# Kernel optimization log

Hardware: AMD Instinct MI355X
Metric: run time of the kernel (lower is better)

Reference implementation:

```python
import jax, jax.numpy as jnp
import numpy as np

B, T, E, H = 64, 256, 300, 512        # batch, longest_sequence, embed dim, hidden
V, NTAGS, NCLS, DFF = 50000, 17, 18, 256  # vocab, universal POS tags, output classes, dense hidden


def setup_inputs() -> dict:
    key = jax.random.key(0)
    ks = jax.random.split(key, 11)
    su = 1.0 / np.sqrt(H)  # PyTorch LSTMCell/Linear uniform init scale
    return {
        "tokens": jax.random.randint(ks[0], (B, T), 0, V),
        "tags": jax.random.randint(ks[1], (T,), 0, NTAGS),
        "emb": jax.random.normal(ks[2], (V, E), jnp.float32),
        "W_ih": jax.random.uniform(ks[3], (NTAGS, 4 * H, E), jnp.float32, -su, su),
        "W_hh": jax.random.uniform(ks[4], (NTAGS, 4 * H, H), jnp.float32, -su, su),
        "b_ih": jax.random.uniform(ks[5], (NTAGS, 4 * H), jnp.float32, -su, su),
        "b_hh": jax.random.uniform(ks[6], (NTAGS, 4 * H), jnp.float32, -su, su),
        "W1": jax.random.uniform(ks[7], (DFF, H), jnp.float32, -su, su),
        "b1": jax.random.uniform(ks[8], (DFF,), jnp.float32, -su, su),
        "W2": jax.random.uniform(ks[9], (NCLS, DFF), jnp.float32, -1.0 / np.sqrt(DFF), 1.0 / np.sqrt(DFF)),
        "b2": jax.random.uniform(ks[10], (NCLS,), jnp.float32, -1.0 / np.sqrt(DFF), 1.0 / np.sqrt(DFF)),
    }


def reference(tokens, tags, emb, W_ih, W_hh, b_ih, b_hh, W1, b1, W2, b2):
    x = emb[tokens]                     # [B, T, E] embedding lookup
    xs = jnp.swapaxes(x, 0, 1)          # [T, B, E] time-major for scan

    def step(carry, inp):
        h, c = carry
        xt, tag = inp                   # xt: [B, E], tag: scalar int routing the cell
        gates = (xt @ W_ih[tag].T + h @ W_hh[tag].T
                 + b_ih[tag] + b_hh[tag])            # [B, 4H]
        i, f, g, o = jnp.split(gates, 4, axis=-1)    # PyTorch LSTMCell gate order
        i = jax.nn.sigmoid(i)
        f = jax.nn.sigmoid(f)
        g = jnp.tanh(g)
        o = jax.nn.sigmoid(o)
        c = f * c + i * g
        h = o * jnp.tanh(c)
        return (h, c), None

    h0 = jnp.zeros((x.shape[0], H), x.dtype)
    (h, _), _ = jax.lax.scan(step, (h0, h0), (xs, tags))
    # dense head: Linear -> ReLU -> (Dropout inactive at eval) -> Linear
    hid = jax.nn.relu(h @ W1.T + b1)
    return hid @ W2.T + b2              # [B, NCLS] multiclass logits
```

## Files before the change

kernel.cpp:

```cpp
#include <hip/hip_runtime.h>
#include <cstdint>
#include <cstddef>

#define BB   64
#define TT   256
#define EE   300
#define HH   512
#define G4H  2048
#define NCLS 18
#define DFF  256
#define NBLK 256

__device__ __forceinline__ float fast_exp2(float x) { return __builtin_amdgcn_exp2f(x); }
__device__ __forceinline__ float sigmoid_f(float x) {
  return 1.0f / (1.0f + fast_exp2(x * -1.442695040888963f));
}
__device__ __forceinline__ float tanh_f(float x) {
  return 2.0f / (1.0f + fast_exp2(x * -2.885390081777927f)) - 1.0f;
}

__global__ __launch_bounds__(256) void xproj_kernel(
    const int* __restrict__ tokens, const int* __restrict__ tags,
    const float* __restrict__ emb, const float* __restrict__ W_ih,
    const float* __restrict__ b_ih, const float* __restrict__ b_hh,
    float* __restrict__ xW, int t0)
{
  const int tid  = threadIdx.x;
  const int lane = tid & 63;
  const int w    = tid >> 6;
  const int rs   = blockIdx.x & 127;
  const int tl   = blockIdx.x >> 7;
  const int t    = t0 + tl;
  const int tag  = tags[t];
  const int row0 = rs * 16;
  const int kbeg = __builtin_amdgcn_readfirstlane(w * 76);
  const bool full = (w != 3);

  const int tok = tokens[lane * TT + t];
  const float* xrow = emb + (size_t)tok * EE + kbeg;
  float xr[76];
  #pragma unroll
  for (int i = 0; i < 18; ++i) {
    const float4 v = *reinterpret_cast<const float4*>(xrow + i * 4);
    xr[i*4+0] = v.x; xr[i*4+1] = v.y; xr[i*4+2] = v.z; xr[i*4+3] = v.w;
  }
  if (full) {
    const float4 v = *reinterpret_cast<const float4*>(xrow + 72);
    xr[72] = v.x; xr[73] = v.y; xr[74] = v.z; xr[75] = v.w;
  } else {
    xr[72] = 0.f; xr[73] = 0.f; xr[74] = 0.f; xr[75] = 0.f;
  }

  const float* Wbase = W_ih + (size_t)tag * ((size_t)G4H * EE);
  __shared__ float red[4][16][64];
  #pragma unroll
  for (int r = 0; r < 16; ++r) {
    const float* Wr = Wbase + (size_t)(row0 + r) * EE + kbeg;
    float a = 0.f;
    #pragma unroll
    for (int k = 0; k < 72; ++k) a = fmaf(Wr[k], xr[k], a);
    if (full) {
      #pragma unroll
      for (int k = 72; k < 76; ++k) a = fmaf(Wr[k], xr[k], a);
    }
    red[w][r][lane] = a;
  }
  __syncthreads();
  #pragma unroll
  for (int it = 0; it < 4; ++it) {
    const int item = tid + it * 256;
    const int r = item >> 6, b = item & 63;
    const int row = row0 + r;
    float s = red[0][r][b] + red[1][r][b] + red[2][r][b] + red[3][r][b];
    s += b_ih[tag * G4H + row] + b_hh[tag * G4H + row];
    xW[((size_t)tl * G4H + row) * BB + b] = s;
  }
}

__global__ __launch_bounds__(1024) void lstm_seq_kernel(
    const int* __restrict__ tags, const float* __restrict__ W_hh,
    const float* __restrict__ xW, float* __restrict__ hA,
    float* __restrict__ hB, float* __restrict__ cst,
    float* __restrict__ hF, unsigned int* __restrict__ flags,
    int t0, int nsteps)
{
  const int tid  = threadIdx.x;
  const int lane = tid & 63;
  const int w    = tid >> 6;
  const int j0   = blockIdx.x * 2;
  const int kbeg = __builtin_amdgcn_readfirstlane(w * 32);

  __shared__ float red[16][8][64];
  __shared__ float gate[8][64];

  const int ejj = tid >> 6, eb = tid & 63;
  const size_t eidx = (size_t)(j0 + ejj) * BB + eb;
  float creg = (tid < 128) ? cst[eidx] : 0.f;

  const int rr = tid >> 6, rb = tid & 63;
  const int rrow = j0 + (rr & 1) + (rr >> 1) * HH;
  float xw_cur = 0.f;
  if (tid < 512) xw_cur = xW[((size_t)0 * G4H + rrow) * BB + rb];

  for (int s = 0; s < nsteps; ++s) {
    const int t   = t0 + s;
    const int tag = tags[t];
    const float* h_in  = (t & 1) ? hB : hA;
    float*       h_out = (t & 1) ? hA : hB;

    float xr[32];
    const float* hp0 = h_in + (size_t)kbeg * BB + lane;
    const float* hp1 = hp0 + 16 * BB;
    asm volatile(
      "global_load_dword %0,  %32, off sc0 sc1\n\t"
      "global_load_dword %1,  %32, off offset:256 sc0 sc1\n\t"
      "global_load_dword %2,  %32, off offset:512 sc0 sc1\n\t"
      "global_load_dword %3,  %32, off offset:768 sc0 sc1\n\t"
      "global_load_dword %4,  %32, off offset:1024 sc0 sc1\n\t"
      "global_load_dword %5,  %32, off offset:1280 sc0 sc1\n\t"
      "global_load_dword %6,  %32, off offset:1536 sc0 sc1\n\t"
      "global_load_dword %7,  %32, off offset:1792 sc0 sc1\n\t"
      "global_load_dword %8,  %32, off offset:2048 sc0 sc1\n\t"
      "global_load_dword %9,  %32, off offset:2304 sc0 sc1\n\t"
      "global_load_dword %10, %32, off offset:2560 sc0 sc1\n\t"
      "global_load_dword %11, %32, off offset:2816 sc0 sc1\n\t"
      "global_load_dword %12, %32, off offset:3072 sc0 sc1\n\t"
      "global_load_dword %13, %32, off offset:3328 sc0 sc1\n\t"
      "global_load_dword %14, %32, off offset:3584 sc0 sc1\n\t"
      "global_load_dword %15, %32, off offset:3840 sc0 sc1\n\t"
      "global_load_dword %16, %33, off sc0 sc1\n\t"
      "global_load_dword %17, %33, off offset:256 sc0 sc1\n\t"
      "global_load_dword %18, %33, off offset:512 sc0 sc1\n\t"
      "global_load_dword %19, %33, off offset:768 sc0 sc1\n\t"
      "global_load_dword %20, %33, off offset:1024 sc0 sc1\n\t"
      "global_load_dword %21, %33, off offset:1280 sc0 sc1\n\t"
      "global_load_dword %22, %33, off offset:1536 sc0 sc1\n\t"
      "global_load_dword %23, %33, off offset:1792 sc0 sc1\n\t"
      "global_load_dword %24, %33, off offset:2048 sc0 sc1\n\t"
      "global_load_dword %25, %33, off offset:2304 sc0 sc1\n\t"
      "global_load_dword %26, %33, off offset:2560 sc0 sc1\n\t"
      "global_load_dword %27, %33, off offset:2816 sc0 sc1\n\t"
      "global_load_dword %28, %33, off offset:3072 sc0 sc1\n\t"
      "global_load_dword %29, %33, off offset:3328 sc0 sc1\n\t"
      "global_load_dword %30, %33, off offset:3584 sc0 sc1\n\t"
      "global_load_dword %31, %33, off offset:3840 sc0 sc1\n\t"
      "s_waitcnt vmcnt(0)"
      : "=&v"(xr[0]),  "=&v"(xr[1]),  "=&v"(xr[2]),  "=&v"(xr[3]),
        "=&v"(xr[4]),  "=&v"(xr[5]),  "=&v"(xr[6]),  "=&v"(xr[7]),
        "=&v"(xr[8]),  "=&v"(xr[9]),  "=&v"(xr[10]), "=&v"(xr[11]),
        "=&v"(xr[12]), "=&v"(xr[13]), "=&v"(xr[14]), "=&v"(xr[15]),
        "=&v"(xr[16]), "=&v"(xr[17]), "=&v"(xr[18]), "=&v"(xr[19]),
        "=&v"(xr[20]), "=&v"(xr[21]), "=&v"(xr[22]), "=&v"(xr[23]),
        "=&v"(xr[24]), "=&v"(xr[25]), "=&v"(xr[26]), "=&v"(xr[27]),
        "=&v"(xr[28]), "=&v"(xr[29]), "=&v"(xr[30]), "=&v"(xr[31])
      : "v"(hp0), "v"(hp1)
      : "memory");

    const float* Wbase = W_hh + (size_t)tag * ((size_t)G4H * HH);
    #pragma unroll
    for (int g = 0; g < 4; ++g) {
      #pragma unroll
      for (int jj = 0; jj < 2; ++jj) {
        const int row = j0 + jj + g * HH;
        const float* Wr = Wbase + (size_t)row * HH + kbeg;
        float a = 0.f;
        #pragma unroll
        for (int k = 0; k < 32; ++k) a = fmaf(Wr[k], xr[k], a);
        red[w][g * 2 + jj][lane] = a;
      }
    }
    __syncthreads();
    if (tid < 512) {
      float sacc = 0.f;
      #pragma unroll
      for (int ww = 0; ww < 16; ++ww) sacc += red[ww][rr][rb];
      gate[rr][rb] = sacc + xw_cur;
    }
    __syncthreads();
    if (tid < 128) {
      const float i_ = sigmoid_f(gate[0 + ejj][eb]);
      const float f_ = sigmoid_f(gate[2 + ejj][eb]);
      const float g_ = tanh_f   (gate[4 + ejj][eb]);
      const float o_ = sigmoid_f(gate[6 + ejj][eb]);
      creg = f_ * creg + i_ * g_;
      const float hval = o_ * tanh_f(creg);
      __hip_atomic_store(&h_out[eidx], hval, __ATOMIC_RELAXED,
                         __HIP_MEMORY_SCOPE_AGENT);
      if (t == TT - 1) hF[eidx] = hval;
    }
    __syncthreads();
    if (s != nsteps - 1) {
      if (tid == 0) {
        __hip_atomic_store(&flags[blockIdx.x * 16], (unsigned int)(s + 1),
                           __ATOMIC_RELAXED, __HIP_MEMORY_SCOPE_AGENT);
      }
      if (tid < 512) xw_cur = xW[((size_t)(s + 1) * G4H + rrow) * BB + rb];
      if (w == 0) {
        const unsigned int target = (unsigned int)(s + 1);
        for (;;) {
          const unsigned int f0 = __hip_atomic_load(&flags[(lane      ) * 16],
                                    __ATOMIC_RELAXED, __HIP_MEMORY_SCOPE_AGENT);
          const unsigned int f1 = __hip_atomic_load(&flags[(lane +  64) * 16],
                                    __ATOMIC_RELAXED, __HIP_MEMORY_SCOPE_AGENT);
          const unsigned int f2 = __hip_atomic_load(&flags[(lane + 128) * 16],
                                    __ATOMIC_RELAXED, __HIP_MEMORY_SCOPE_AGENT);
          const unsigned int f3 = __hip_atomic_load(&flags[(lane + 192) * 16],
                                    __ATOMIC_RELAXED, __HIP_MEMORY_SCOPE_AGENT);
          if (__all(f0 >= target && f1 >= target && f2 >= target && f3 >= target))
            break;
        }
      }
      __syncthreads();
    }
  }
  if (tid < 128) cst[eidx] = creg;
}

__global__ __launch_bounds__(1024) void head1_kernel(
    const float* __restrict__ W1, const float* __restrict__ b1,
    const float* __restrict__ hfin, float* __restrict__ hid)
{
  const int tid  = threadIdx.x;
  const int lane = tid & 63;
  const int w    = tid >> 6;
  const int row0 = blockIdx.x * 8;
  const int kbeg = __builtin_amdgcn_readfirstlane(w * 32);
  float xr[32];
  const float* hp = hfin + (size_t)kbeg * BB + lane;
  #pragma unroll
  for (int i = 0; i < 32; ++i) xr[i] = hp[i * BB];
  __shared__ float red[16][8][64];
  #pragma unroll
  for (int r = 0; r < 8; ++r) {
    const float* Wr = W1 + (size_t)(row0 + r) * HH + kbeg;
    float a = 0.f;
    #pragma unroll
    for (int k = 0; k < 32; ++k) a = fmaf(Wr[k], xr[k], a);
    red[w][r][lane] = a;
  }
  __syncthreads();
  if (tid < 512) {
    const int r = tid >> 6, b = tid & 63;
    float s = 0.f;
    #pragma unroll
    for (int ww = 0; ww < 16; ++ww) s += red[ww][r][b];
    s += b1[row0 + r];
    hid[(size_t)(row0 + r) * BB + b] = fmaxf(s, 0.f);
  }
}

__global__ __launch_bounds__(256) void head2_kernel(
    const float* __restrict__ W2, const float* __restrict__ b2,
    const float* __restrict__ hid, float* __restrict__ out)
{
  const int tid  = threadIdx.x;
  const int lane = tid & 63;
  const int w    = tid >> 6;
  const int kbeg = __builtin_amdgcn_readfirstlane(w * 64);
  float xr[64];
  const float* hp = hid + (size_t)kbeg * BB + lane;
  #pragma unroll
  for (int i = 0; i < 64; ++i) xr[i] = hp[i * BB];
  __shared__ float red[4][NCLS][64];
  #pragma unroll
  for (int r = 0; r < NCLS; ++r) {
    const float* Wr = W2 + (size_t)r * DFF + kbeg;
    float a = 0.f;
    #pragma unroll
    for (int k = 0; k < 64; ++k) a = fmaf(Wr[k], xr[k], a);
    red[w][r][lane] = a;
  }
  __syncthreads();
  for (int it = 0; it < 5; ++it) {
    const int item = tid + it * 256;
    if (item < NCLS * 64) {
      const int r = item >> 6, b = item & 63;
      float s = red[0][r][b] + red[1][r][b] + red[2][r][b] + red[3][r][b];
      out[(size_t)b * NCLS + r] = s + b2[r];
    }
  }
}

extern "C" void kernel_launch(void* const* d_in, const int* in_sizes, int n_in,
                              void* d_out, int out_size, void* d_ws, size_t ws_size,
                              hipStream_t stream)
{
  const int*   tokens = (const int*)  d_in[0];
  const int*   tags   = (const int*)  d_in[1];
  const float* emb    = (const float*)d_in[2];
  const float* W_ih   = (const float*)d_in[3];
  const float* W_hh   = (const float*)d_in[4];
  const float* b_ih   = (const float*)d_in[5];
  const float* b_hh   = (const float*)d_in[6];
  const float* W1     = (const float*)d_in[7];
  const float* b1     = (const float*)d_in[8];
  const float* W2     = (const float*)d_in[9];
  const float* b2     = (const float*)d_in[10];
  float* out = (float*)d_out;

  const size_t per_t = (size_t)G4H * BB * sizeof(float);
  int TCH = 8;
  for (int c = 256; c >= 8; c >>= 1) {
    if ((size_t)c * per_t + (4u << 20) <= ws_size) { TCH = c; break; }
  }
  char* p = (char*)d_ws;
  float* xW  = (float*)p;  p += (size_t)TCH * per_t;
  float* hA  = (float*)p;  p += (size_t)HH * BB * sizeof(float);
  float* hB  = (float*)p;  p += (size_t)HH * BB * sizeof(float);
  float* cst = (float*)p;  p += (size_t)HH * BB * sizeof(float);
  float* hF  = (float*)p;  p += (size_t)HH * BB * sizeof(float);
  float* hid = (float*)p;  p += (size_t)DFF * BB * sizeof(float);
  unsigned int* flags = (unsigned int*)p;

  (void)hipMemsetAsync(hA,  0, (size_t)HH * BB * sizeof(float), stream);
  (void)hipMemsetAsync(cst, 0, (size_t)HH * BB * sizeof(float), stream);

  for (int c0 = 0; c0 < TT; c0 += TCH) {
    xproj_kernel<<<dim3((unsigned)TCH * 128), dim3(256), 0, stream>>>(
        tokens, tags, emb, W_ih, b_ih, b_hh, xW, c0);
    (void)hipMemsetAsync(flags, 0, NBLK * 16 * sizeof(unsigned int), stream);
    {
      int t0 = c0, nsteps = TCH;
      void* args[] = { (void*)&tags, (void*)&W_hh, (void*)&xW,
                       (void*)&hA, (void*)&hB, (void*)&cst, (void*)&hF,
                       (void*)&flags, (void*)&t0, (void*)&nsteps };
      hipLaunchCooperativeKernel((const void*)lstm_seq_kernel,
                                 dim3(NBLK), dim3(1024), args, 0, stream);
    }
  }
  head1_kernel<<<dim3(32), dim3(1024), 0, stream>>>(W1, b1, hF, hid);
  head2_kernel<<<dim3(1), dim3(256), 0, stream>>>(W2, b2, hid, out);
}
```

Baseline: 2.256 ms.

## Double-buffer next step's W_hh rows in shared memory via prefetch

```diff
diff --git a/kernel.cpp b/kernel.cpp
--- a/kernel.cpp
+++ b/kernel.cpp
@@ -92,6 +92,7 @@
 
   __shared__ float red[16][8][64];
   __shared__ float gate[8][64];
+  __shared__ float wbuf[2][8][512];
 
   const int ejj = tid >> 6, eb = tid & 63;
   const size_t eidx = (size_t)(j0 + ejj) * BB + eb;
@@ -102,9 +103,22 @@
   float xw_cur = 0.f;
   if (tid < 512) xw_cur = xW[((size_t)0 * G4H + rrow) * BB + rb];
 
+  const int pr  = w >> 1;
+  const int phb = w & 1;
+  const size_t prow_off = (size_t)(j0 + (pr & 1) + (pr >> 1) * HH) * HH
+                          + phb * 256 + lane * 4;
+
+  {
+    const int tag0 = tags[t0];
+    const float4 w0 = *reinterpret_cast<const float4*>(
+        W_hh + (size_t)tag0 * ((size_t)G4H * HH) + prow_off);
+    *reinterpret_cast<float4*>(&wbuf[0][pr][phb * 256 + lane * 4]) = w0;
+  }
+  __syncthreads();
+
   for (int s = 0; s < nsteps; ++s) {
     const int t   = t0 + s;
-    const int tag = tags[t];
+    const int cur = s & 1;
     const float* h_in  = (t & 1) ? hB : hA;
     float*       h_out = (t & 1) ? hA : hB;
 
@@ -156,20 +170,38 @@
       : "v"(hp0), "v"(hp1)
       : "memory");
 
-    const float* Wbase = W_hh + (size_t)tag * ((size_t)G4H * HH);
+    const bool pre = (s + 1 < nsteps);
+    float4 wpre;
+    if (pre) {
+      const int ntag = tags[t + 1];
+      wpre = *reinterpret_cast<const float4*>(
+          W_hh + (size_t)ntag * ((size_t)G4H * HH) + prow_off);
+    }
+
     #pragma unroll
     for (int g = 0; g < 4; ++g) {
       #pragma unroll
       for (int jj = 0; jj < 2; ++jj) {
-        const int row = j0 + jj + g * HH;
-        const float* Wr = Wbase + (size_t)row * HH + kbeg;
+        const int r = g * 2 + jj;
+        const float* Wr = &wbuf[cur][r][kbeg];
         float a = 0.f;
         #pragma unroll
-        for (int k = 0; k < 32; ++k) a = fmaf(Wr[k], xr[k], a);
-        red[w][g * 2 + jj][lane] = a;
+        for (int i = 0; i < 8; ++i) {
+          const float4 wv = *reinterpret_cast<const float4*>(Wr + i * 4);
+          a = fmaf(wv.x, xr[i*4+0], a);
+          a = fmaf(wv.y, xr[i*4+1], a);
+          a = fmaf(wv.z, xr[i*4+2], a);
+          a = fmaf(wv.w, xr[i*4+3], a);
+        }
+        red[w][r][lane] = a;
       }
     }
+
+    if (pre) {
+      *reinterpret_cast<float4*>(&wbuf[cur ^ 1][pr][phb * 256 + lane * 4]) = wpre;
+    }
     __syncthreads();
+
     if (tid < 512) {
       float sacc = 0.f;
       #pragma unroll
```

After: 1.864 ms. -17.4%, faster.
